# Optimization experiments

Measured on AMD Instinct MI355X. Metric: run time of the kernel, lower is better.

## Reference

```python
import jax, jax.numpy as jnp
import numpy as np

H, C = 4, 32          # num_heads, hidden_channels
NEG_ATT = 0.2         # GAT attention leaky_relu slope (PyG default)
NEG_ACT = 0.01        # F.leaky_relu default slope applied after each conv


def gat_conv(x_src, x_dst, Wsrc, Wdst, a_src, a_dst, bias, src_idx, dst_idx, n_dst):
    """One bipartite GATConv (add_self_loops=False, concat=True)."""
    hs = (x_src @ Wsrc).reshape(-1, H, C)            # [Ns,H,C]
    hd = (x_dst @ Wdst).reshape(-1, H, C)            # [Nd,H,C]
    a_s = (hs * a_src).sum(-1)                       # [Ns,H]
    a_d = (hd * a_dst).sum(-1)                       # [Nd,H]
    e = jax.nn.leaky_relu(a_s[src_idx] + a_d[dst_idx], NEG_ATT)  # [E,H]
    m = jax.ops.segment_max(e, dst_idx, num_segments=n_dst)      # [Nd,H]
    ex = jnp.exp(e - m[dst_idx])
    denom = jax.ops.segment_sum(ex, dst_idx, num_segments=n_dst)
    alpha = ex / (denom[dst_idx] + 1e-16)            # edge softmax over dst
    msg = hs[src_idx] * alpha[:, :, None]            # [E,H,C]
    out = jax.ops.segment_sum(msg, dst_idx, num_segments=n_dst)  # [Nd,H,C]
    return out.reshape(n_dst, H * C) + bias


def setup_inputs() -> dict:
    key = jax.random.key(0)
    ks = jax.random.split(key, 40)
    it = iter(range(40))
    Nu, Nm, E, D, O = 100000, 20000, 500000, 64, 64
    HC = H * C

    def rn(shape, s=0.1):
        return jax.random.normal(ks[next(it)], shape, jnp.float32) * s

    def ri(n, hi):
        return jax.random.randint(ks[next(it)], (n,), 0, hi)

    return {
        "user_ids": jnp.arange(Nu), "movie_ids": jnp.arange(Nm),
        "um_src": ri(E, Nu), "um_dst": ri(E, Nm),
        "mu_src": ri(E, Nm), "mu_dst": ri(E, Nu),
        "user_emb": rn((Nu, D)), "movie_emb": rn((Nm, D)),
        "l1_um_Wsrc": rn((D, HC)), "l1_um_Wdst": rn((D, HC)),
        "l1_um_asrc": rn((H, C)), "l1_um_adst": rn((H, C)), "l1_um_b": rn((HC,)),
        "l1_mu_Wsrc": rn((D, HC)), "l1_mu_Wdst": rn((D, HC)),
        "l1_mu_asrc": rn((H, C)), "l1_mu_adst": rn((H, C)), "l1_mu_b": rn((HC,)),
        "l2_um_W": rn((HC, HC)), "l2_um_asrc": rn((H, C)), "l2_um_adst": rn((H, C)), "l2_um_b": rn((HC,)),
        "l2_mu_W": rn((HC, HC)), "l2_mu_asrc": rn((H, C)), "l2_mu_adst": rn((H, C)), "l2_mu_b": rn((HC,)),
        "Wo": rn((HC, O)), "bo": rn((O,)),
    }


def reference(user_ids, movie_ids, um_src, um_dst, mu_src, mu_dst,
              user_emb, movie_emb,
              l1_um_Wsrc, l1_um_Wdst, l1_um_asrc, l1_um_adst, l1_um_b,
              l1_mu_Wsrc, l1_mu_Wdst, l1_mu_asrc, l1_mu_adst, l1_mu_b,
              l2_um_W, l2_um_asrc, l2_um_adst, l2_um_b,
              l2_mu_W, l2_mu_asrc, l2_mu_adst, l2_mu_b,
              Wo, bo):
    xu = user_emb[user_ids]
    xm = movie_emb[movie_ids]
    Nu, Nm = xu.shape[0], xm.shape[0]
    # layer 1 (HeteroConv sum: each dst type receives exactly one edge type here)
    hm = gat_conv(xu, xm, l1_um_Wsrc, l1_um_Wdst, l1_um_asrc, l1_um_adst, l1_um_b, um_src, um_dst, Nm)
    hu = gat_conv(xm, xu, l1_mu_Wsrc, l1_mu_Wdst, l1_mu_asrc, l1_mu_adst, l1_mu_b, mu_src, mu_dst, Nu)
    xu = jax.nn.leaky_relu(hu, NEG_ACT)
    xm = jax.nn.leaky_relu(hm, NEG_ACT)
    # layer 2 (non-bipartite in_channels int => shared lin for src and dst)
    hm = gat_conv(xu, xm, l2_um_W, l2_um_W, l2_um_asrc, l2_um_adst, l2_um_b, um_src, um_dst, Nm)
    hu = gat_conv(xm, xu, l2_mu_W, l2_mu_W, l2_mu_asrc, l2_mu_adst, l2_mu_b, mu_src, mu_dst, Nu)
    xu = jax.nn.leaky_relu(hu, NEG_ACT)
    xm = jax.nn.leaky_relu(hm, NEG_ACT)
    out_user = xu @ Wo + bo
    out_movie = xm @ Wo + bo
    return out_user, out_movie, xu, xm
```

## Files before the change

kernel.cpp:

```cpp
#include <hip/hip_runtime.h>
#include <hip/hip_bf16.h>
#include <cstdint>


#define HC 128
#define HH 4
#define WPART 256
#define EPB 2048

typedef __attribute__((ext_vector_type(8))) short bf16x8;
typedef __attribute__((ext_vector_type(4))) float f32x4;

__device__ __forceinline__ short f2bf(float f) {
    return __builtin_bit_cast(short, __float2bfloat16(f));
}
__device__ __forceinline__ float bf2f(ushort u) {
    return __builtin_bit_cast(float, ((unsigned)u) << 16);
}

struct VT { const float* W[8]; const float* a[8]; float* v[8]; };
__global__ void make_v_all_k(VT t) {
    int gid = blockIdx.x * 256 + threadIdx.x;
    int task, base;
    if (gid < 1024) { task = gid >> 8; base = gid & 255; }
    else if (gid < 3072) { int g = gid - 1024; task = 4 + (g >> 9); base = g & 511; }
    else return;
    int k = base >> 2, h = base & 3;
    int coff = (task & 1) * 4;
    const float* wr = t.W[task] + (size_t)k * HC + h * 32;
    const float* ar = t.a[task] + h * 32;
    float s = 0.f;
    #pragma unroll
    for (int c = 0; c < 32; ++c) s = fmaf(wr[c], ar[c], s);
    t.v[task][k * 8 + coff + h] = s;
}

struct PT { const float* W[5]; const float* V[5]; ushort* Wb[5];
            int K[5]; int Nw[5]; int start[6]; };
__global__ void pack_all_k(PT t) {
    int gid = blockIdx.x * 256 + threadIdx.x;
    if (gid >= t.start[5]) return;
    int task = 0;
    while (gid >= t.start[task + 1]) ++task;
    int loc = gid - t.start[task];
    int K = t.K[task], Nw = t.Nw[task];
    int n = loc / K, k = loc % K;
    float v = 0.f;
    if (n < Nw) v = t.W[task][(size_t)k * Nw + n];
    else if (t.V[task] != nullptr && n < Nw + 8) v = t.V[task][k * 8 + (n - Nw)];
    t.Wb[task][loc] = (ushort)f2bf(v);
}

template <int NT, int MODE, bool ABF>
__global__ __launch_bounds__(256) void gemm_dual_k(
    const void* A0, const int* idx0, const ushort* Wb0, ushort* hsb0,
    ushort* atts0, float* attd0, float* C0, const float* bias0, int M0, int nb0,
    const void* A1, const int* idx1, const ushort* Wb1, ushort* hsb1,
    ushort* atts1, float* attd1, float* C1, const float* bias1, int M1,
    int K, int ldc) {
    const void* A; const int* aidx; const ushort* Wb; ushort* hsb;
    ushort* atts; float* attd; float* C; const float* bias; int M, bid;
    if ((int)blockIdx.x < nb0) {
        A = A0; aidx = idx0; Wb = Wb0; hsb = hsb0; atts = atts0; attd = attd0;
        C = C0; bias = bias0; M = M0; bid = blockIdx.x;
    } else {
        A = A1; aidx = idx1; Wb = Wb1; hsb = hsb1; atts = atts1; attd = attd1;
        C = C1; bias = bias1; M = M1; bid = blockIdx.x - nb0;
    }
    int lane = threadIdx.x & 63;
    int wave = threadIdx.x >> 6;
    int m_base = bid * 128 + wave * 32;
    int lm = lane & 15;
    int kg = lane >> 4;

    int r0 = m_base + lm, r1 = r0 + 16;
    int cr0 = r0 < M ? r0 : M - 1;
    int cr1 = r1 < M ? r1 : M - 1;
    int row0 = aidx ? aidx[cr0] : cr0;
    int row1 = aidx ? aidx[cr1] : cr1;
    const ushort* bp = Wb + (size_t)lm * K + kg * 8;

    f32x4 acc[2][NT] = {};
    for (int k0 = 0; k0 < K; k0 += 32) {
        bf16x8 a[2];
        if (ABF) {
            const ushort* a0p = (const ushort*)A + (size_t)row0 * K + kg * 8;
            const ushort* a1p = (const ushort*)A + (size_t)row1 * K + kg * 8;
            a[0] = *reinterpret_cast<const bf16x8*>(a0p + k0);
            a[1] = *reinterpret_cast<const bf16x8*>(a1p + k0);
        } else {
            const float* a0p = (const float*)A + (size_t)row0 * K + kg * 8;
            const float* a1p = (const float*)A + (size_t)row1 * K + kg * 8;
            float af[2][8];
            *reinterpret_cast<float4*>(&af[0][0]) = *reinterpret_cast<const float4*>(a0p + k0);
            *reinterpret_cast<float4*>(&af[0][4]) = *reinterpret_cast<const float4*>(a0p + k0 + 4);
            *reinterpret_cast<float4*>(&af[1][0]) = *reinterpret_cast<const float4*>(a1p + k0);
            *reinterpret_cast<float4*>(&af[1][4]) = *reinterpret_cast<const float4*>(a1p + k0 + 4);
            #pragma unroll
            for (int mi = 0; mi < 2; ++mi)
                #pragma unroll
                for (int j = 0; j < 8; ++j) a[mi][j] = f2bf(af[mi][j]);
        }
        #pragma unroll
        for (int nt = 0; nt < NT; ++nt) {
            bf16x8 b = *reinterpret_cast<const bf16x8*>(bp + (size_t)nt * 16 * K + k0);
            acc[0][nt] = __builtin_amdgcn_mfma_f32_16x16x32_bf16(a[0], b, acc[0][nt], 0, 0, 0);
            acc[1][nt] = __builtin_amdgcn_mfma_f32_16x16x32_bf16(a[1], b, acc[1][nt], 0, 0, 0);
        }
    }
    #pragma unroll
    for (int mi = 0; mi < 2; ++mi) {
        int rowb = m_base + mi * 16 + kg * 4;
        if (MODE == 0) {
            #pragma unroll
            for (int nt = 0; nt < NT - 1; ++nt) {
                int col = nt * 16 + lm;
                #pragma unroll
                for (int r = 0; r < 4; ++r) {
                    int row = rowb + r;
                    if (row < M) hsb[(size_t)row * HC + col] = (ushort)f2bf(acc[mi][nt][r]);
                }
            }
            #pragma unroll
            for (int r = 0; r < 4; ++r) {
                int row = rowb + r;
                if (row < M) {
                    float v = acc[mi][NT - 1][r];
                    if (lm < 4) atts[(size_t)row * 4 + lm] = (ushort)f2bf(v);
                    else if (lm < 8) attd[(size_t)row * 4 + (lm - 4)] = v;
                }
            }
        } else {
            #pragma unroll
            for (int nt = 0; nt < NT; ++nt) {
                int col = nt * 16 + lm;
                float bv = bias[col];
                #pragma unroll
                for (int r = 0; r < 4; ++r) {
                    int row = rowb + r;
                    if (row < M) C[(size_t)row * ldc + col] = acc[mi][nt][r] + bv;
                }
            }
        }
    }
}

__global__ __launch_bounds__(256) void part_count_k(
    const int* __restrict__ d0, int E0,
    const int* __restrict__ d1, int E1, int Nm,
    int* __restrict__ cntmat, int NB1) {
    __shared__ int lh[WPART];
    int t = threadIdx.x;
    lh[t] = 0;
    __syncthreads();
    int base = blockIdx.x * EPB + t;
    #pragma unroll
    for (int j = 0; j < EPB / 256; ++j) {
        int e = base + j * 256;
        int key = -1;
        if (e < E0) key = d0[e];
        else if (e - E0 < E1) key = Nm + d1[e - E0];
        if (key >= 0) atomicAdd(&lh[key >> 9], 1);
    }
    __syncthreads();
    cntmat[(size_t)t * NB1 + blockIdx.x] = lh[t];
}

__global__ __launch_bounds__(256) void part_scatter_k(
    const int* __restrict__ s0, const int* __restrict__ d0, int E0,
    const int* __restrict__ s1, const int* __restrict__ d1, int E1, int Nm,
    const int* __restrict__ scanned, int NB1, int2* __restrict__ buf) {
    __shared__ int lb[WPART];
    __shared__ int lc[WPART];
    int t = threadIdx.x;
    lb[t] = scanned[(size_t)t * NB1 + blockIdx.x];
    lc[t] = 0;
    __syncthreads();
    int base = blockIdx.x * EPB + t;
    #pragma unroll
    for (int j = 0; j < EPB / 256; ++j) {
        int e = base + j * 256;
        int key = -1, src = 0;
        if (e < E0) { key = d0[e]; src = s0[e]; }
        else if (e - E0 < E1) { key = Nm + d1[e - E0]; src = s1[e - E0]; }
        if (key >= 0) {
            int w = key >> 9;
            int r = atomicAdd(&lc[w], 1);
            buf[lb[w] + r] = make_int2(src, key);
        }
    }
}

__global__ __launch_bounds__(512) void csort_k(
    const int2* __restrict__ buf, const int* __restrict__ scanned, int NB1,
    int E, int NK, int* __restrict__ rs, int* __restrict__ csr) {
    __shared__ int c1[512];
    __shared__ int ls[512];
    int b = blockIdx.x;
    int t = threadIdx.x;
    int lo = scanned[(size_t)b * NB1];
    int hi = (b + 1 < WPART) ? scanned[(size_t)(b + 1) * NB1] : E;
    int keylo = b << 9;
    c1[t] = 0;
    __syncthreads();
    for (int i = lo + t; i < hi; i += 512)
        atomicAdd(&c1[buf[i].y - keylo], 1);
    __syncthreads();
    int v = c1[t];
    ls[t] = v;
    __syncthreads();
    for (int off = 1; off < 512; off <<= 1) {
        int x = (t >= off) ? ls[t - off] : 0;
        __syncthreads();
        ls[t] += x;
        __syncthreads();
    }
    ls[t] -= v;
    int gk = keylo + t;
    if (gk <= NK) rs[gk] = lo + ls[t];
    c1[t] = 0;
    __syncthreads();
    for (int i = lo + t; i < hi; i += 512) {
        int2 p = buf[i];
        int k = p.y - keylo;
        int r = atomicAdd(&c1[k], 1);
        csr[lo + ls[k] + r] = p.x;
    }
}

__global__ void scan_block_k(const int* __restrict__ deg, int n,
                             int* __restrict__ out, int* __restrict__ partial) {
    __shared__ int s[256];
    int i = blockIdx.x * 256 + threadIdx.x;
    int v = (i < n) ? deg[i] : 0;
    s[threadIdx.x] = v;
    __syncthreads();
    for (int off = 1; off < 256; off <<= 1) {
        int x = (threadIdx.x >= off) ? s[threadIdx.x - off] : 0;
        __syncthreads();
        s[threadIdx.x] += x;
        __syncthreads();
    }
    if (i < n) out[i] = s[threadIdx.x] - v;
    if (threadIdx.x == 255) partial[blockIdx.x] = s[255];
}

__global__ void scan_partial_k(int* __restrict__ partial, int nb) {
    __shared__ int s[512];
    int t = threadIdx.x;
    int v = (t < nb) ? partial[t] : 0;
    s[t] = v;
    __syncthreads();
    for (int off = 1; off < 512; off <<= 1) {
        int x = (t >= off) ? s[t - off] : 0;
        __syncthreads();
        s[t] += x;
        __syncthreads();
    }
    if (t < nb) partial[t] = s[t] - v;
}

__global__ void add_off_k(int* __restrict__ out, const int* __restrict__ partial, int n) {
    int i = blockIdx.x * 256 + threadIdx.x;
    if (i < n) out[i] += partial[blockIdx.x];
}

template <bool WF32, bool WBF, bool PROJ>
__global__ __launch_bounds__(256) void agg16_dual_k(
    const int* __restrict__ rs0, const int* __restrict__ csr0,
    const ushort* __restrict__ hsb0, const ushort* __restrict__ atts0,
    const float* __restrict__ attd0, const float* __restrict__ bias0,
    float* __restrict__ out0, ushort* __restrict__ outb0, int n0,
    const int* __restrict__ rs1, const int* __restrict__ csr1,
    const ushort* __restrict__ hsb1, const ushort* __restrict__ atts1,
    const float* __restrict__ attd1, const float* __restrict__ bias1,
    float* __restrict__ out1, ushort* __restrict__ outb1, int n1,
    const ushort* __restrict__ Wbo, const float* __restrict__ bo,
    float* __restrict__ pj0, float* __restrict__ pj1) {
    int g = (int)((blockIdx.x * 256u + threadIdx.x) >> 4);
    int gl = (threadIdx.x >> 4) & 15;
    const int* rs; const int* csr; const ushort* hsb; const ushort* atts;
    const float* attd; const float* bias; float* out; ushort* outb;
    int node; bool active = true;
    if (g < n0) {
        rs = rs0; csr = csr0; hsb = hsb0; atts = atts0; attd = attd0;
        bias = bias0; out = out0; outb = outb0; node = g;
    } else {
        node = g - n0;
        if (node >= n1) { active = false; node = 0; }
        rs = rs1; csr = csr1; hsb = hsb1; atts = atts1; attd = attd1;
        bias = bias1; out = out1; outb = outb1;
    }
    int c = threadIdx.x & 15;
    int h = c >> 2;
    float ad = attd[node * 4 + h];
    int s0 = 0, s1 = 0;
    if (active) { s0 = rs[node]; s1 = rs[node + 1]; }
    float acc[8] = {};
    float wsum = 0.f;
    int i = s0;
    for (; i + 4 <= s1; i += 4) {
        int sx[4];
        #pragma unroll
        for (int j = 0; j < 4; ++j) sx[j] = csr[i + j];
        bf16x8 hv[4]; float el[4];
        #pragma unroll
        for (int j = 0; j < 4; ++j) {
            hv[j] = *reinterpret_cast<const bf16x8*>(hsb + (size_t)sx[j] * HC + 8 * c);
            el[j] = bf2f(atts[(size_t)sx[j] * 4 + h]);
        }
        #pragma unroll
        for (int j = 0; j < 4; ++j) {
            float e = el[j] + ad;
            e = e > 0.f ? e : 0.2f * e;
            float w = __expf(e);
            wsum += w;
            #pragma unroll
            for (int k = 0; k < 8; ++k)
                acc[k] = fmaf(w, bf2f((ushort)hv[j][k]), acc[k]);
        }
    }
    for (; i < s1; ++i) {
        int src = csr[i];
        bf16x8 hv = *reinterpret_cast<const bf16x8*>(hsb + (size_t)src * HC + 8 * c);
        float e = bf2f(atts[(size_t)src * 4 + h]) + ad;
        e = e > 0.f ? e : 0.2f * e;
        float w = __expf(e);
        wsum += w;
        #pragma unroll
        for (int k = 0; k < 8; ++k)
            acc[k] = fmaf(w, bf2f((ushort)hv[k]), acc[k]);
    }
    float inv = 1.f / (wsum + 1e-16f);
    float v[8];
    #pragma unroll
    for (int k = 0; k < 8; ++k) {
        v[k] = fmaf(acc[k], inv, bias[8 * c + k]);
        v[k] = v[k] > 0.f ? v[k] : 0.01f * v[k];
    }
    if (active && WF32) {
        float4 o0 = make_float4(v[0], v[1], v[2], v[3]);
        float4 o1 = make_float4(v[4], v[5], v[6], v[7]);
        reinterpret_cast<float4*>(out + (size_t)node * HC + 8 * c)[0] = o0;
        reinterpret_cast<float4*>(out + (size_t)node * HC + 8 * c)[1] = o1;
    }
    if (active && WBF) {
        bf16x8 u;
        #pragma unroll
        for (int k = 0; k < 8; ++k) u[k] = f2bf(v[k]);
        *reinterpret_cast<bf16x8*>(outb + (size_t)node * HC + 8 * c) = u;
    }
    if constexpr (PROJ) {
        __shared__ ushort As[16][136];
        bf16x8 u;
        #pragma unroll
        for (int k = 0; k < 8; ++k) u[k] = active ? f2bf(v[k]) : (short)0;
        *reinterpret_cast<bf16x8*>(&As[gl][8 * c]) = u;
        __syncthreads();
        int lane = threadIdx.x & 63;
        int wv = threadIdx.x >> 6;
        int lm = lane & 15;
        int kg = lane >> 4;
        int col = wv * 16 + lm;
        const ushort* bp = Wbo + (size_t)col * HC + kg * 8;
        f32x4 pacc = {};
        #pragma unroll
        for (int k0 = 0; k0 < HC; k0 += 32) {
            bf16x8 a = *reinterpret_cast<const bf16x8*>(&As[lm][k0 + kg * 8]);
            bf16x8 b = *reinterpret_cast<const bf16x8*>(bp + k0);
            pacc = __builtin_amdgcn_mfma_f32_16x16x32_bf16(a, b, pacc, 0, 0, 0);
        }
        float bv = bo[col];
        int blockBase = blockIdx.x * 16;
        #pragma unroll
        for (int r = 0; r < 4; ++r) {
            int slot = kg * 4 + r;
            int ng = blockBase + slot;
            if (ng < n0) pj0[(size_t)ng * 64 + col] = pacc[r] + bv;
            else if (ng - n0 < n1) pj1[(size_t)(ng - n0) * 64 + col] = pacc[r] + bv;
        }
    }
}

extern "C" void kernel_launch(void* const* d_in, const int* in_sizes, int n_in,
                              void* d_out, int out_size, void* d_ws, size_t ws_size,
                              hipStream_t stream) {
    const int Nu = in_sizes[0];
    const int Nm = in_sizes[1];
    const int E1 = in_sizes[2];
    const int E2 = in_sizes[4];
    const int D  = in_sizes[6] / Nu;
    const int O  = in_sizes[27];
    const int E  = E1 + E2;
    const int NK = Nm + Nu;

    const int*   user_ids  = (const int*)d_in[0];
    const int*   movie_ids = (const int*)d_in[1];
    const int*   um_src    = (const int*)d_in[2];
    const int*   um_dst    = (const int*)d_in[3];
    const int*   mu_src    = (const int*)d_in[4];
    const int*   mu_dst    = (const int*)d_in[5];
    const float* user_emb  = (const float*)d_in[6];
    const float* movie_emb = (const float*)d_in[7];
    const float* l1_um_Wsrc = (const float*)d_in[8];
    const float* l1_um_Wdst = (const float*)d_in[9];
    const float* l1_um_asrc = (const float*)d_in[10];
    const float* l1_um_adst = (const float*)d_in[11];
    const float* l1_um_b    = (const float*)d_in[12];
    const float* l1_mu_Wsrc = (const float*)d_in[13];
    const float* l1_mu_Wdst = (const float*)d_in[14];
    const float* l1_mu_asrc = (const float*)d_in[15];
    const float* l1_mu_adst = (const float*)d_in[16];
    const float* l1_mu_b    = (const float*)d_in[17];
    const float* l2_um_W    = (const float*)d_in[18];
    const float* l2_um_asrc = (const float*)d_in[19];
    const float* l2_um_adst = (const float*)d_in[20];
    const float* l2_um_b    = (const float*)d_in[21];
    const float* l2_mu_W    = (const float*)d_in[22];
    const float* l2_mu_asrc = (const float*)d_in[23];
    const float* l2_mu_adst = (const float*)d_in[24];
    const float* l2_mu_b    = (const float*)d_in[25];
    const float* Wo         = (const float*)d_in[26];
    const float* bo         = (const float*)d_in[27];

    auto cdiv = [](int a, int b) { return (a + b - 1) / b; };
    const int NB1 = cdiv(E, EPB);
    const int CM  = WPART * NB1;

    char* p = (char*)d_ws;
    auto alloc = [&](size_t bytes) { void* r = p; p += (bytes + 255) & ~(size_t)255; return r; };
    ushort* hs_u = (ushort*)alloc((size_t)Nu * HC * 2);
    ushort* hs_m = (ushort*)alloc((size_t)Nm * HC * 2);
    ushort* XUb  = (ushort*)alloc((size_t)Nu * HC * 2);
    ushort* XMb  = (ushort*)alloc((size_t)Nm * HC * 2);
    ushort* atts_u = (ushort*)alloc((size_t)Nu * 4 * 2);
    ushort* atts_m = (ushort*)alloc((size_t)Nm * 4 * 2);
    float* attd_u = (float*)alloc((size_t)Nu * 4 * 4);
    float* attd_m = (float*)alloc((size_t)Nm * 4 * 4);
    float* V_u1  = (float*)alloc((size_t)HC * 8 * 4);
    float* V_m1  = (float*)alloc((size_t)HC * 8 * 4);
    float* V_u2  = (float*)alloc((size_t)HC * 8 * 4);
    float* V_m2  = (float*)alloc((size_t)HC * 8 * 4);
    ushort* Wb_u1 = (ushort*)alloc((size_t)144 * D * 2);
    ushort* Wb_m1 = (ushort*)alloc((size_t)144 * D * 2);
    ushort* Wb_u2 = (ushort*)alloc((size_t)144 * HC * 2);
    ushort* Wb_m2 = (ushort*)alloc((size_t)144 * HC * 2);
    ushort* Wb_o  = (ushort*)alloc((size_t)64 * HC * 2);
    int* rs      = (int*)alloc((size_t)(NK + 2) * 4);
    int* cntmat  = (int*)alloc((size_t)(CM + 256) * 4);
    int* scanned = (int*)alloc((size_t)(CM + 256) * 4);
    int2* buf    = (int2*)alloc((size_t)E * 8);
    int* csr     = (int*)alloc((size_t)E * 4);
    int* part    = (int*)alloc(1024 * 4);

    {
        VT vt;
        const float* Ws[8] = {l1_um_Wsrc, l1_mu_Wdst, l1_mu_Wsrc, l1_um_Wdst,
                              l2_um_W, l2_mu_W, l2_mu_W, l2_um_W};
        const float* as[8] = {l1_um_asrc, l1_mu_adst, l1_mu_asrc, l1_um_adst,
                              l2_um_asrc, l2_mu_adst, l2_mu_asrc, l2_um_adst};
        float* vs[8] = {V_u1, V_u1, V_m1, V_m1, V_u2, V_u2, V_m2, V_m2};
        for (int i = 0; i < 8; ++i) { vt.W[i] = Ws[i]; vt.a[i] = as[i]; vt.v[i] = vs[i]; }
        make_v_all_k<<<12, 256, 0, stream>>>(vt);

        PT pt;
        const float* pW[5] = {l1_um_Wsrc, l1_mu_Wsrc, l2_um_W, l2_mu_W, Wo};
        const float* pV[5] = {V_u1, V_m1, V_u2, V_m2, nullptr};
        ushort* pB[5] = {Wb_u1, Wb_m1, Wb_u2, Wb_m2, Wb_o};
        int pK[5] = {D, D, HC, HC, HC};
        int pN[5] = {HC, HC, HC, HC, 64};
        int cum = 0;
        for (int i = 0; i < 5; ++i) {
            pt.W[i] = pW[i]; pt.V[i] = pV[i]; pt.Wb[i] = pB[i];
            pt.K[i] = pK[i]; pt.Nw[i] = pN[i];
            pt.start[i] = cum;
            cum += (i < 4 ? 144 : 64) * pK[i];
        }
        pt.start[5] = cum;
        pack_all_k<<<cdiv(cum, 256), 256, 0, stream>>>(pt);
    }

    part_count_k<<<NB1, 256, 0, stream>>>(um_dst, E1, mu_dst, E2, Nm, cntmat, NB1);
    {
        int nb = cdiv(CM, 256);
        scan_block_k<<<nb, 256, 0, stream>>>(cntmat, CM, scanned, part);
        scan_partial_k<<<1, 512, 0, stream>>>(part, nb);
        add_off_k<<<nb, 256, 0, stream>>>(scanned, part, CM);
    }
    part_scatter_k<<<NB1, 256, 0, stream>>>(um_src, um_dst, E1, mu_src, mu_dst, E2,
                                            Nm, scanned, NB1, buf);
    csort_k<<<WPART, 512, 0, stream>>>(buf, scanned, NB1, E, NK, rs, csr);

    float* OU = (float*)d_out;
    float* OM = OU + (size_t)Nu * O;
    float* XU = OM + (size_t)Nm * O;
    float* XM = XU + (size_t)Nu * HC;

    int gbU = cdiv(Nu, 128), gbM = cdiv(Nm, 128);
    int aggBlocks = cdiv((Nm + Nu) * 16, 256);

    gemm_dual_k<9, 0, false><<<gbU + gbM, 256, 0, stream>>>(
        user_emb, user_ids, Wb_u1, hs_u, atts_u, attd_u, nullptr, nullptr, Nu, gbU,
        movie_emb, movie_ids, Wb_m1, hs_m, atts_m, attd_m, nullptr, nullptr, Nm,
        D, 0);
    agg16_dual_k<false, true, false><<<aggBlocks, 256, 0, stream>>>(
        rs, csr, hs_u, atts_u, attd_m, l1_um_b, nullptr, XMb, Nm,
        rs + Nm, csr, hs_m, atts_m, attd_u, l1_mu_b, nullptr, XUb, Nu,
        nullptr, nullptr, nullptr, nullptr);

    gemm_dual_k<9, 0, true><<<gbU + gbM, 256, 0, stream>>>(
        XUb, nullptr, Wb_u2, hs_u, atts_u, attd_u, nullptr, nullptr, Nu, gbU,
        XMb, nullptr, Wb_m2, hs_m, atts_m, attd_m, nullptr, nullptr, Nm,
        HC, 0);
    agg16_dual_k<true, false, true><<<aggBlocks, 256, 0, stream>>>(
        rs, csr, hs_u, atts_u, attd_m, l2_um_b, XM, nullptr, Nm,
        rs + Nm, csr, hs_m, atts_m, attd_u, l2_mu_b, XU, nullptr, Nu,
        Wb_o, bo, OM, OU);
}
```

Baseline: 209.0 us.

## Fuse layer-2 projection GEMM into layer-1 aggregation epilogue

```diff
diff --git a/kernel.cpp b/kernel.cpp
--- a/kernel.cpp
+++ b/kernel.cpp
@@ -265,37 +265,42 @@
     if (i < n) out[i] += partial[blockIdx.x];
 }
 
-template <bool WF32, bool WBF, bool PROJ>
+template <bool WF32, bool PROJ, bool GEMM2>
 __global__ __launch_bounds__(256) void agg16_dual_k(
     const int* __restrict__ rs0, const int* __restrict__ csr0,
     const ushort* __restrict__ hsb0, const ushort* __restrict__ atts0,
     const float* __restrict__ attd0, const float* __restrict__ bias0,
-    float* __restrict__ out0, ushort* __restrict__ outb0, int n0,
+    float* __restrict__ out0, int n0,
     const int* __restrict__ rs1, const int* __restrict__ csr1,
     const ushort* __restrict__ hsb1, const ushort* __restrict__ atts1,
     const float* __restrict__ attd1, const float* __restrict__ bias1,
-    float* __restrict__ out1, ushort* __restrict__ outb1, int n1,
+    float* __restrict__ out1, int n1,
     const ushort* __restrict__ Wbo, const float* __restrict__ bo,
-    float* __restrict__ pj0, float* __restrict__ pj1) {
-    int g = (int)((blockIdx.x * 256u + threadIdx.x) >> 4);
-    int gl = (threadIdx.x >> 4) & 15;
-    const int* rs; const int* csr; const ushort* hsb; const ushort* atts;
-    const float* attd; const float* bias; float* out; ushort* outb;
-    int node; bool active = true;
-    if (g < n0) {
-        rs = rs0; csr = csr0; hsb = hsb0; atts = atts0; attd = attd0;
-        bias = bias0; out = out0; outb = outb0; node = g;
-    } else {
-        node = g - n0;
-        if (node >= n1) { active = false; node = 0; }
-        rs = rs1; csr = csr1; hsb = hsb1; atts = atts1; attd = attd1;
-        bias = bias1; out = out1; outb = outb1;
-    }
-    int c = threadIdx.x & 15;
-    int h = c >> 2;
-    float ad = attd[node * 4 + h];
+    float* __restrict__ pj0, float* __restrict__ pj1,
+    const ushort* __restrict__ W2_0, ushort* __restrict__ hs2_0,
+    ushort* __restrict__ atts2_0, float* __restrict__ attd2_0,
+    const ushort* __restrict__ W2_1, ushort* __restrict__ hs2_1,
+    ushort* __restrict__ atts2_1, float* __restrict__ attd2_1) {
+    int blocksM = (n0 + 15) >> 4;
+    bool ty1 = (int)blockIdx.x >= blocksM;
+    int base = ty1 ? ((int)blockIdx.x - blocksM) * 16 : (int)blockIdx.x * 16;
+    int gl = threadIdx.x >> 4;
+    int c  = threadIdx.x & 15;
+    int h  = c >> 2;
+    const int* rs = ty1 ? rs1 : rs0;
+    const int* csr = ty1 ? csr1 : csr0;
+    const ushort* hsb = ty1 ? hsb1 : hsb0;
+    const ushort* atts = ty1 ? atts1 : atts0;
+    const float* attd = ty1 ? attd1 : attd0;
+    const float* bias = ty1 ? bias1 : bias0;
+    int n = ty1 ? n1 : n0;
+    int node = base + gl;
+    bool active = node < n;
+    int nodeC = active ? node : 0;
+
+    float ad = attd[nodeC * 4 + h];
     int s0 = 0, s1 = 0;
-    if (active) { s0 = rs[node]; s1 = rs[node + 1]; }
+    if (active) { s0 = rs[nodeC]; s1 = rs[nodeC + 1]; }
     float acc[8] = {};
     float wsum = 0.f;
     int i = s0;
@@ -338,19 +343,14 @@
         v[k] = fmaf(acc[k], inv, bias[8 * c + k]);
         v[k] = v[k] > 0.f ? v[k] : 0.01f * v[k];
     }
-    if (active && WF32) {
+    if (WF32 && active) {
+        float* out = ty1 ? out1 : out0;
         float4 o0 = make_float4(v[0], v[1], v[2], v[3]);
         float4 o1 = make_float4(v[4], v[5], v[6], v[7]);
         reinterpret_cast<float4*>(out + (size_t)node * HC + 8 * c)[0] = o0;
         reinterpret_cast<float4*>(out + (size_t)node * HC + 8 * c)[1] = o1;
     }
-    if (active && WBF) {
-        bf16x8 u;
-        #pragma unroll
-        for (int k = 0; k < 8; ++k) u[k] = f2bf(v[k]);
-        *reinterpret_cast<bf16x8*>(outb + (size_t)node * HC + 8 * c) = u;
-    }
-    if constexpr (PROJ) {
+    if constexpr (PROJ || GEMM2) {
         __shared__ ushort As[16][136];
         bf16x8 u;
         #pragma unroll
@@ -361,23 +361,55 @@
         int wv = threadIdx.x >> 6;
         int lm = lane & 15;
         int kg = lane >> 4;
-        int col = wv * 16 + lm;
-        const ushort* bp = Wbo + (size_t)col * HC + kg * 8;
-        f32x4 pacc = {};
-        #pragma unroll
-        for (int k0 = 0; k0 < HC; k0 += 32) {
-            bf16x8 a = *reinterpret_cast<const bf16x8*>(&As[lm][k0 + kg * 8]);
-            bf16x8 b = *reinterpret_cast<const bf16x8*>(bp + k0);
-            pacc = __builtin_amdgcn_mfma_f32_16x16x32_bf16(a, b, pacc, 0, 0, 0);
-        }
-        float bv = bo[col];
-        int blockBase = blockIdx.x * 16;
-        #pragma unroll
-        for (int r = 0; r < 4; ++r) {
-            int slot = kg * 4 + r;
-            int ng = blockBase + slot;
-            if (ng < n0) pj0[(size_t)ng * 64 + col] = pacc[r] + bv;
-            else if (ng - n0 < n1) pj1[(size_t)(ng - n0) * 64 + col] = pacc[r] + bv;
+        if constexpr (PROJ) {
+            int col = wv * 16 + lm;
+            const ushort* bp = Wbo + (size_t)col * HC + kg * 8;
+            f32x4 pacc = {};
+            #pragma unroll
+            for (int k0 = 0; k0 < HC; k0 += 32) {
+                bf16x8 a = *reinterpret_cast<const bf16x8*>(&As[lm][k0 + kg * 8]);
+                bf16x8 b = *reinterpret_cast<const bf16x8*>(bp + k0);
+                pacc = __builtin_amdgcn_mfma_f32_16x16x32_bf16(a, b, pacc, 0, 0, 0);
+            }
+            float bv = bo[col];
+            float* pj = ty1 ? pj1 : pj0;
+            #pragma unroll
+            for (int r = 0; r < 4; ++r) {
+                int nd = base + kg * 4 + r;
+                if (nd < n) pj[(size_t)nd * 64 + col] = pacc[r] + bv;
+            }
+        }
+        if constexpr (GEMM2) {
+            const ushort* W2 = ty1 ? W2_1 : W2_0;
+            ushort* hs2 = ty1 ? hs2_1 : hs2_0;
+            ushort* atts2 = ty1 ? atts2_1 : atts2_0;
+            float* attd2 = ty1 ? attd2_1 : attd2_0;
+            #pragma unroll
+            for (int ti = 0; ti < 3; ++ti) {
+                int t = wv + ti * 4;
+                if (t > 8) break;
+                int col = t * 16 + lm;
+                const ushort* bp = W2 + (size_t)col * HC + kg * 8;
+                f32x4 gacc = {};
+                #pragma unroll
+                for (int k0 = 0; k0 < HC; k0 += 32) {
+                    bf16x8 a = *reinterpret_cast<const bf16x8*>(&As[lm][k0 + kg * 8]);
+                    bf16x8 b = *reinterpret_cast<const bf16x8*>(bp + k0);
+                    gacc = __builtin_amdgcn_mfma_f32_16x16x32_bf16(a, b, gacc, 0, 0, 0);
+                }
+                #pragma unroll
+                for (int r = 0; r < 4; ++r) {
+                    int nd = base + kg * 4 + r;
+                    if (nd < n) {
+                        if (t < 8) {
+                            hs2[(size_t)nd * HC + col] = (ushort)f2bf(gacc[r]);
+                        } else {
+                            if (lm < 4) atts2[(size_t)nd * 4 + lm] = (ushort)f2bf(gacc[r]);
+                            else if (lm < 8) attd2[(size_t)nd * 4 + (lm - 4)] = gacc[r];
+                        }
+                    }
+                }
+            }
         }
     }
 }
@@ -429,14 +461,18 @@
 
     char* p = (char*)d_ws;
     auto alloc = [&](size_t bytes) { void* r = p; p += (bytes + 255) & ~(size_t)255; return r; };
-    ushort* hs_u = (ushort*)alloc((size_t)Nu * HC * 2);
-    ushort* hs_m = (ushort*)alloc((size_t)Nm * HC * 2);
-    ushort* XUb  = (ushort*)alloc((size_t)Nu * HC * 2);
-    ushort* XMb  = (ushort*)alloc((size_t)Nm * HC * 2);
-    ushort* atts_u = (ushort*)alloc((size_t)Nu * 4 * 2);
-    ushort* atts_m = (ushort*)alloc((size_t)Nm * 4 * 2);
-    float* attd_u = (float*)alloc((size_t)Nu * 4 * 4);
-    float* attd_m = (float*)alloc((size_t)Nm * 4 * 4);
+    ushort* hs_u  = (ushort*)alloc((size_t)Nu * HC * 2);
+    ushort* hs_m  = (ushort*)alloc((size_t)Nm * HC * 2);
+    ushort* hs_u2 = (ushort*)alloc((size_t)Nu * HC * 2);
+    ushort* hs_m2 = (ushort*)alloc((size_t)Nm * HC * 2);
+    ushort* atts_u  = (ushort*)alloc((size_t)Nu * 4 * 2);
+    ushort* atts_m  = (ushort*)alloc((size_t)Nm * 4 * 2);
+    ushort* atts_u2 = (ushort*)alloc((size_t)Nu * 4 * 2);
+    ushort* atts_m2 = (ushort*)alloc((size_t)Nm * 4 * 2);
+    float* attd_u  = (float*)alloc((size_t)Nu * 4 * 4);
+    float* attd_m  = (float*)alloc((size_t)Nm * 4 * 4);
+    float* attd_u2 = (float*)alloc((size_t)Nu * 4 * 4);
+    float* attd_m2 = (float*)alloc((size_t)Nm * 4 * 4);
     float* V_u1  = (float*)alloc((size_t)HC * 8 * 4);
     float* V_m1  = (float*)alloc((size_t)HC * 8 * 4);
     float* V_u2  = (float*)alloc((size_t)HC * 8 * 4);
@@ -497,23 +533,23 @@
     float* XM = XU + (size_t)Nu * HC;
 
     int gbU = cdiv(Nu, 128), gbM = cdiv(Nm, 128);
-    int aggBlocks = cdiv((Nm + Nu) * 16, 256);
+    int aggBlocks = cdiv(Nm, 16) + cdiv(Nu, 16);
 
     gemm_dual_k<9, 0, false><<<gbU + gbM, 256, 0, stream>>>(
         user_emb, user_ids, Wb_u1, hs_u, atts_u, attd_u, nullptr, nullptr, Nu, gbU,
         movie_emb, movie_ids, Wb_m1, hs_m, atts_m, attd_m, nullptr, nullptr, Nm,
         D, 0);
-    agg16_dual_k<false, true, false><<<aggBlocks, 256, 0, stream>>>(
-        rs, csr, hs_u, atts_u, attd_m, l1_um_b, nullptr, XMb, Nm,
-        rs + Nm, csr, hs_m, atts_m, attd_u, l1_mu_b, nullptr, XUb, Nu,
+    agg16_dual_k<false, false, true><<<aggBlocks, 256, 0, stream>>>(
+        rs, csr, hs_u, atts_u, attd_m, l1_um_b, nullptr, Nm,
+        rs + Nm, csr, hs_m, atts_m, attd_u, l1_mu_b, nullptr, Nu,
+        nullptr, nullptr, nullptr, nullptr,
+        Wb_m2, hs_m2, atts_m2, attd_m2,
+        Wb_u2, hs_u2, atts_u2, attd_u2);
+
+    agg16_dual_k<true, true, false><<<aggBlocks, 256, 0, stream>>>(
+        rs, csr, hs_u2, atts_u2, attd_m2, l2_um_b, XM, Nm,
+        rs + Nm, csr, hs_m2, atts_m2, attd_u2, l2_mu_b, XU, Nu,
+        Wb_o, bo, OM, OU,
+        nullptr, nullptr, nullptr, nullptr,
         nullptr, nullptr, nullptr, nullptr);
-
-    gemm_dual_k<9, 0, true><<<gbU + gbM, 256, 0, stream>>>(
-        XUb, nullptr, Wb_u2, hs_u, atts_u, attd_u, nullptr, nullptr, Nu, gbU,
-        XMb, nullptr, Wb_m2, hs_m, atts_m, attd_m, nullptr, nullptr, Nm,
-        HC, 0);
-    agg16_dual_k<true, false, true><<<aggBlocks, 256, 0, stream>>>(
-        rs, csr, hs_u, atts_u, attd_m, l2_um_b, XM, nullptr, Nm,
-        rs + Nm, csr, hs_m, atts_m, attd_u, l2_mu_b, XU, nullptr, Nu,
-        Wb_o, bo, OM, OU);
-}
+}
```

New measurement: 204.1 us (median of 2 runs). 1.02x faster.
